# Performance work log

Hardware: AMD Instinct MI355X
Metric: run time of the kernel (lower is better)

## Reference

```python
import jax, jax.numpy as jnp
import numpy as np

B, F, L, P, H = 32, 64, 8192, 96, 8
HD = F // H
EPS_ATTN = 1e-6
EPS_REVIN = 1e-5
EPS_LN = 1e-5


def setup_inputs() -> dict:
    key = jax.random.key(0)
    ks = jax.random.split(key, 8)
    f32 = jnp.float32
    return {
        'x': jax.random.normal(ks[0], (B, F, L), dtype=f32),
        'gamma': jnp.ones((1, 1, F), dtype=f32),
        'beta': jnp.zeros((1, 1, F), dtype=f32),
        'ln_w': jnp.ones((F,), dtype=f32),
        'ln_b': jnp.zeros((F,), dtype=f32),
        'Wq': 0.05 * jax.random.normal(ks[1], (F, F), dtype=f32),
        'bq': jnp.zeros((F,), dtype=f32),
        'Wk': 0.05 * jax.random.normal(ks[2], (F, F), dtype=f32),
        'bk': jnp.zeros((F,), dtype=f32),
        'Wv': 0.05 * jax.random.normal(ks[3], (F, F), dtype=f32),
        'bv': jnp.zeros((F,), dtype=f32),
        'Wo': 0.05 * jax.random.normal(ks[4], (F, F), dtype=f32),
        'bo': jnp.zeros((F,), dtype=f32),
        'Wlin': 0.01 * jax.random.normal(ks[5], (P, L), dtype=f32),
        'blin': jnp.zeros((P,), dtype=f32),
        'Wp': 0.1 * jax.random.normal(ks[6], (1, F), dtype=f32),
        'bp': jnp.zeros((1,), dtype=f32),
    }


def _phi(t):
    # feature map: elu(x) + 1 (non-negative)
    return jax.nn.elu(t) + 1.0


def _layernorm(h, w, b):
    mu = jnp.mean(h, axis=-1, keepdims=True)
    var = jnp.mean(jnp.square(h - mu), axis=-1, keepdims=True)
    return (h - mu) * jax.lax.rsqrt(var + EPS_LN) * w + b


def reference(x, gamma, beta, ln_w, ln_b, Wq, bq, Wk, bk, Wv, bv, Wo, bo,
              Wlin, blin, Wp, bp):
    # (B, F, L) -> (B, L, F)
    xt = jnp.transpose(x, (0, 2, 1))
    # RevIN norm (stats over time axis, detached; torch std is unbiased ddof=1)
    mean = jax.lax.stop_gradient(jnp.mean(xt, axis=1, keepdims=True))
    std = jax.lax.stop_gradient(jnp.std(xt, axis=1, keepdims=True, ddof=1) + EPS_REVIN)
    xn = (xt - mean) / std * gamma + beta
    residual = xn
    h = _layernorm(xn, ln_w, ln_b)
    # Q/K/V projections (torch Linear: h @ W.T + b)
    Q = h @ Wq.T + bq
    K = h @ Wk.T + bk
    V = h @ Wv.T + bv
    # (B, L, F) -> (B, H, L, HD)
    def heads(t):
        return jnp.transpose(t.reshape(B, L, H, HD), (0, 2, 1, 3))
    Q, K, V = heads(Q), heads(K), heads(V)
    Q, K = _phi(Q), _phi(K)
    # linear attention: phi(Q) (phi(K)^T V) / (phi(Q) sum_n phi(K))
    KV = jnp.einsum('bhnd,bhne->bhde', K, V)           # (B,H,HD,HD)
    out = jnp.einsum('bhnd,bhde->bhne', Q, KV)          # (B,H,L,HD)
    Z = jnp.sum(K, axis=2)                              # (B,H,HD)
    normalizer = jnp.einsum('bhnd,bhd->bhn', Q, Z)[..., None] + EPS_ATTN
    out = out / normalizer
    out = jnp.transpose(out, (0, 2, 1, 3)).reshape(B, L, F)
    out = out @ Wo.T + bo
    y = out + residual                                  # (B, L, F)
    # temporal linear: (B, F, L) @ Wlin.T -> (B, F, P) -> (B, P, F)
    y = jnp.transpose(jnp.transpose(y, (0, 2, 1)) @ Wlin.T + blin, (0, 2, 1))
    # RevIN denorm
    y = (y - beta) / gamma
    y = y * std + mean
    # projector to scalar per step
    return (y @ Wp.T + bp)[..., 0]                      # (B, P)
```

## Files before the change

### kernel.cpp

```cpp
#include <hip/hip_runtime.h>
#include <cstddef>

#define NB 32
#define NF 64
#define NL 8192
#define NP 96
#define NH 8
#define TSPLIT 16

#define WS_MEAN 0
#define WS_STD  2048
#define WS_RSTD 4096
#define WS_KV   6144
#define WS_Z    22528
#define WS_OUT2 24576
#define WS_MUN  221184
#define WS_RSN  483328
#define WS_WLB  745472
#define WS_XNB  1138688
#define WS_YT   9527296
#define WS_XB   17915904

typedef __bf16 bfx8 __attribute__((ext_vector_type(8)));
typedef float f32x4 __attribute__((ext_vector_type(4)));
#define MFMA16(a, b, c) __builtin_amdgcn_mfma_f32_16x16x32_bf16((a), (b), (c), 0, 0, 0)

__device__ __forceinline__ unsigned short f2bf(float f) {
  unsigned u = __float_as_uint(f);
  unsigned r = u + 0x7FFFu + ((u >> 16) & 1u);
  return (unsigned short)(r >> 16);
}
__device__ __forceinline__ unsigned packbf2(float lo, float hi) {
  return (unsigned)f2bf(lo) | ((unsigned)f2bf(hi) << 16);
}
__device__ __forceinline__ float bflo(unsigned d) { return __uint_as_float(d << 16); }
__device__ __forceinline__ float bfhi(unsigned d) { return __uint_as_float(d & 0xFFFF0000u); }
__device__ __forceinline__ float bf1(unsigned short s) { return __uint_as_float(((unsigned)s) << 16); }

__device__ __forceinline__ bfx8 ldfrag(const unsigned short* p) {
  uint4 u = *(const uint4*)p;
  return __builtin_bit_cast(bfx8, u);
}

__global__ __launch_bounds__(256) void k_stats(const float* __restrict__ x,
                                               float* __restrict__ wmean,
                                               float* __restrict__ wstd,
                                               float* __restrict__ wrstd,
                                               unsigned short* __restrict__ xb) {
  int bf = blockIdx.x;
  int tid = threadIdx.x;
  const float4* row4 = (const float4*)(x + (size_t)bf * NL);
  unsigned short* xrow = xb + (size_t)bf * NL;
  float s1 = 0.f, s2 = 0.f;
#pragma unroll
  for (int i = 0; i < NL / 4 / 256; i++) {
    float4 v = row4[tid + i * 256];
    s1 += v.x + v.y + v.z + v.w;
    s2 += v.x * v.x + v.y * v.y + v.z * v.z + v.w * v.w;
    uint2 o;
    o.x = packbf2(v.x, v.y);
    o.y = packbf2(v.z, v.w);
    *(uint2*)&xrow[(tid + i * 256) * 4] = o;
  }
  __shared__ float r1[256], r2[256];
  r1[tid] = s1; r2[tid] = s2;
  __syncthreads();
  for (int off = 128; off > 0; off >>= 1) {
    if (tid < off) { r1[tid] += r1[tid + off]; r2[tid] += r2[tid + off]; }
    __syncthreads();
  }
  if (tid == 0) {
    float m = r1[0] * (1.f / NL);
    float var = (r2[0] - (float)NL * m * m) * (1.f / (NL - 1));
    float sd = sqrtf(fmaxf(var, 0.f)) + 1e-5f;
    wmean[bf] = m;
    wstd[bf] = sd;
    wrstd[bf] = 1.f / sd;
  }
}

__global__ __launch_bounds__(256) void k_wlb(const float* __restrict__ Wlin,
                                             unsigned short* __restrict__ wlb) {
  int i = blockIdx.x * 256 + threadIdx.x;
  int p = i >> 10;
  int l8 = (i & 1023) * 8;
  float4 va = *(const float4*)&Wlin[(size_t)p * NL + l8];
  float4 vb = *(const float4*)&Wlin[(size_t)p * NL + l8 + 4];
  uint4 o;
  o.x = packbf2(va.x, va.y); o.y = packbf2(va.z, va.w);
  o.z = packbf2(vb.x, vb.y); o.w = packbf2(vb.z, vb.w);
  *(uint4*)&wlb[(((size_t)(l8 >> 5)) * NP + p) * 32 + (l8 & 31)] = o;
}

__global__ __launch_bounds__(256, 4) void k_kv(
    const unsigned short* __restrict__ xb,
    const float* __restrict__ gamma, const float* __restrict__ beta,
    const float* __restrict__ lnw, const float* __restrict__ lnb,
    const float* __restrict__ Wk, const float* __restrict__ bk,
    const float* __restrict__ Wv, const float* __restrict__ bv,
    const float* __restrict__ wmean, const float* __restrict__ wrstd,
    float* __restrict__ wKV, float* __restrict__ wZ,
    float* __restrict__ wmun, float* __restrict__ wrsn,
    unsigned short* __restrict__ xnb) {
  __shared__ __align__(16) char smem[40960];
  unsigned short* hA  = (unsigned short*)smem;
  unsigned short* WkB = (unsigned short*)(smem + 18432);
  unsigned short* WvB = (unsigned short*)(smem + 27648);
  unsigned short* pK  = (unsigned short*)smem;
  unsigned short* pV  = (unsigned short*)(smem + 17408);
  float* SkT   = (float*)(smem + 36864);
  float* mun   = (float*)(smem + 37888);
  float* rsn   = (float*)(smem + 38400);
  float* pmom  = (float*)(smem + 38912);

  const int tid = threadIdx.x;
  const int b = blockIdx.x >> 6;
  const int tI = blockIdx.x & 63;
  const int L0 = tI * 128;
  const int lane = tid & 63, wv = tid >> 6;
  const int mm = lane & 15, qd = lane >> 4;

  {
    int jj = tid >> 2, g = tid & 3;
    int f0 = g * 16;
    float tkp = 0.f, tvp = 0.f;
#pragma unroll
    for (int i = 0; i < 4; i++) {
      int f = f0 + i * 4;
      float4 wk4 = *(const float4*)&Wk[jj * NF + f];
      float4 wv4 = *(const float4*)&Wv[jj * NF + f];
      float4 lw  = *(const float4*)&lnw[f];
      float4 lb  = *(const float4*)&lnb[f];
      uint2 pk2, pv2;
      pk2.x = packbf2(wk4.x * lw.x, wk4.y * lw.y);
      pk2.y = packbf2(wk4.z * lw.z, wk4.w * lw.w);
      pv2.x = packbf2(wv4.x * lw.x, wv4.y * lw.y);
      pv2.y = packbf2(wv4.z * lw.z, wv4.w * lw.w);
      *(uint2*)&WkB[jj * 72 + f] = pk2;
      *(uint2*)&WvB[jj * 72 + f] = pv2;
      tkp += lb.x * wk4.x + lb.y * wk4.y + lb.z * wk4.z + lb.w * wk4.w;
      tvp += lb.x * wv4.x + lb.y * wv4.y + lb.z * wv4.z + lb.w * wv4.w;
    }
    tkp += __shfl_xor(tkp, 1, 64); tkp += __shfl_xor(tkp, 2, 64);
    tvp += __shfl_xor(tvp, 1, 64); tvp += __shfl_xor(tvp, 2, 64);
    if (g == 0) {
      SkT[64 + jj]  = tkp + bk[jj];
      SkT[192 + jj] = tvp + bv[jj];
    }
  }

  {
    const int sel = tid >> 7;
    const int l = tid & 127;
    const int fbase = sel * 32;
    float s1 = 0.f, s2 = 0.f;
    float xn2[32];
#pragma unroll
    for (int i = 0; i < 32; i++) {
      int f = fbase + i;
      float v = bf1(xb[((size_t)(b * NF + f)) * NL + L0 + l]);
      v = (v - wmean[b * NF + f]) * wrstd[b * NF + f] * gamma[f] + beta[f];
      xn2[i] = v; s1 += v; s2 += v * v;
    }
    pmom[sel * 256 + l * 2] = s1;
    pmom[sel * 256 + l * 2 + 1] = s2;
    unsigned* hrow = (unsigned*)&hA[l * 72];
#pragma unroll
    for (int i = 0; i < 16; i++)
      hrow[fbase / 2 + i] = packbf2(xn2[2 * i], xn2[2 * i + 1]);
  }
  __syncthreads();

  if (tid < 128) {
    float s1 = pmom[tid * 2] + pmom[256 + tid * 2];
    float s2 = pmom[tid * 2 + 1] + pmom[256 + tid * 2 + 1];
    float mu = s1 * (1.f / NF);
    float var = s2 * (1.f / NF) - mu * mu;
    float rs = rsqrtf(fmaxf(var, 0.f) + 1e-5f);
    mun[tid] = mu; rsn[tid] = rs;
    wmun[(size_t)b * NL + L0 + tid] = mu;
    wrsn[(size_t)b * NL + L0 + tid] = rs;
  } else {
    int sel = (tid >> 6) - 2, j = tid & 63;
    const unsigned* wr = (const unsigned*)((sel ? WvB : WkB) + j * 72);
    float s = 0.f;
#pragma unroll
    for (int i = 0; i < 32; i++) { unsigned d = wr[i]; s += bflo(d) + bfhi(d); }
    SkT[sel * 128 + j] = s;
  }

  {
    int row = tid >> 1, half = tid & 1;
    const uint4* s4 = (const uint4*)&hA[row * 72 + half * 32];
    uint4* d4 = (uint4*)(xnb + (((size_t)(b * 64 + tI) * 128 + row) * 64 + half * 32));
    d4[0] = s4[0]; d4[1] = s4[1]; d4[2] = s4[2]; d4[3] = s4[3];
  }
  __syncthreads();

  const f32x4 fz = {0.f, 0.f, 0.f, 0.f};
  f32x4 kacc[2][4], vacc[2][4];
#pragma unroll
  for (int i = 0; i < 2; i++)
#pragma unroll
    for (int jt = 0; jt < 4; jt++) { kacc[i][jt] = fz; vacc[i][jt] = fz; }

#pragma unroll
  for (int kc = 0; kc < 2; kc++) {
    bfx8 a0 = ldfrag(&hA[(wv * 32 + mm) * 72 + kc * 32 + qd * 8]);
    bfx8 a1 = ldfrag(&hA[(wv * 32 + 16 + mm) * 72 + kc * 32 + qd * 8]);
#pragma unroll
    for (int jt = 0; jt < 4; jt++) {
      bfx8 bkf = ldfrag(&WkB[(jt * 16 + mm) * 72 + kc * 32 + qd * 8]);
      bfx8 bvf = ldfrag(&WvB[(jt * 16 + mm) * 72 + kc * 32 + qd * 8]);
      kacc[0][jt] = MFMA16(a0, bkf, kacc[0][jt]);
      kacc[1][jt] = MFMA16(a1, bkf, kacc[1][jt]);
      vacc[0][jt] = MFMA16(a0, bvf, vacc[0][jt]);
      vacc[1][jt] = MFMA16(a1, bvf, vacc[1][jt]);
    }
  }

#pragma unroll
  for (int lt2 = 0; lt2 < 2; lt2++) {
    float4 mu4 = *(const float4*)&mun[wv * 32 + lt2 * 16 + qd * 4];
    float4 rs4 = *(const float4*)&rsn[wv * 32 + lt2 * 16 + qd * 4];
    float muv[4] = {mu4.x, mu4.y, mu4.z, mu4.w};
    float rsv[4] = {rs4.x, rs4.y, rs4.z, rs4.w};
#pragma unroll
    for (int jt = 0; jt < 4; jt++) {
      int j = jt * 16 + mm;
      float Sk = SkT[j], Tk = SkT[64 + j], Sv = SkT[128 + j], Tv = SkT[192 + j];
#pragma unroll
      for (int r = 0; r < 4; r++) {
        float kk = rsv[r] * (kacc[lt2][jt][r] - muv[r] * Sk) + Tk;
        kacc[lt2][jt][r] = (kk > 0.f) ? (kk + 1.f) : __expf(kk);
        vacc[lt2][jt][r] = rsv[r] * (vacc[lt2][jt][r] - muv[r] * Sv) + Tv;
      }
    }
  }
  __syncthreads();

#pragma unroll
  for (int lt2 = 0; lt2 < 2; lt2++) {
    int l0 = wv * 32 + lt2 * 16 + qd * 4;
#pragma unroll
    for (int jt = 0; jt < 4; jt++) {
      int j = jt * 16 + mm;
      uint2 dk, dv;
      dk.x = packbf2(kacc[lt2][jt][0], kacc[lt2][jt][1]);
      dk.y = packbf2(kacc[lt2][jt][2], kacc[lt2][jt][3]);
      dv.x = packbf2(vacc[lt2][jt][0], vacc[lt2][jt][1]);
      dv.y = packbf2(vacc[lt2][jt][2], vacc[lt2][jt][3]);
      *(uint2*)&pK[j * 136 + l0] = dk;
      *(uint2*)&pV[j * 136 + l0] = dv;
    }
  }
  __syncthreads();

  {
    f32x4 racc = fz;
#pragma unroll
    for (int kb = 0; kb < 4; kb++) {
      bfx8 ak = ldfrag(&pK[(wv * 16 + mm) * 136 + kb * 32 + qd * 8]);
      bfx8 bv8 = ldfrag(&pV[(wv * 16 + mm) * 136 + kb * 32 + qd * 8]);
      racc = MFMA16(ak, bv8, racc);
    }
    int eh = mm >> 3, e = mm & 7;
#pragma unroll
    for (int r = 0; r < 4; r++) {
      int row = qd * 4 + r;
      if ((row >> 3) == eh)
        atomicAdd(&wKV[(b * NH + wv * 2 + eh) * 64 + (row & 7) * 8 + e], racc[r]);
    }
  }
  if (tid < 64) {
    const unsigned* kr = (const unsigned*)&pK[tid * 136];
    float zs = 0.f;
#pragma unroll
    for (int i = 0; i < 64; i++) { unsigned d = kr[i]; zs += bflo(d) + bfhi(d); }
    atomicAdd(&wZ[b * 64 + tid], zs);
  }
}

__global__ __launch_bounds__(256, 4) void k_qy(
    const unsigned short* __restrict__ xnb,
    const float* __restrict__ lnw, const float* __restrict__ lnb,
    const float* __restrict__ Wq, const float* __restrict__ bq,
    const float* __restrict__ Wo, const float* __restrict__ bo,
    const float* __restrict__ wmun, const float* __restrict__ wrsn,
    const float* __restrict__ wKV, const float* __restrict__ wZ,
    unsigned short* __restrict__ ytb) {
  __shared__ __align__(16) char smem[40704];
  unsigned short* hA  = (unsigned short*)smem;
  unsigned short* qaA = (unsigned short*)smem;
  unsigned short* WqB = (unsigned short*)(smem + 18432);
  unsigned short* WoB = (unsigned short*)(smem + 27648);
  float* kvz   = (float*)(smem + 36864);
  float* mun   = (float*)(smem + 39168);
  float* rsn   = (float*)(smem + 39680);
  float* SqTq  = (float*)(smem + 40192);

  const int tid = threadIdx.x;
  const int b = blockIdx.x >> 6;
  const int tI = blockIdx.x & 63;
  const int L0 = tI * 128;
  const int lane = tid & 63, wv = tid >> 6;
  const int mm = lane & 15, qd = lane >> 4;
  const unsigned short* xtile = xnb + (size_t)(b * 64 + tI) * 128 * 64;

  {
    int jj = tid >> 2, g = tid & 3;
    int f0 = g * 16;
    float tqp = 0.f;
#pragma unroll
    for (int i = 0; i < 4; i++) {
      int f = f0 + i * 4;
      float4 wq4 = *(const float4*)&Wq[jj * NF + f];
      float4 wo4 = *(const float4*)&Wo[jj * NF + f];
      float4 lw  = *(const float4*)&lnw[f];
      float4 lb  = *(const float4*)&lnb[f];
      uint2 pq2, po2;
      pq2.x = packbf2(wq4.x * lw.x, wq4.y * lw.y);
      pq2.y = packbf2(wq4.z * lw.z, wq4.w * lw.w);
      po2.x = packbf2(wo4.x, wo4.y);
      po2.y = packbf2(wo4.z, wo4.w);
      *(uint2*)&WqB[jj * 72 + f] = pq2;
      *(uint2*)&WoB[jj * 72 + f] = po2;
      tqp += lb.x * wq4.x + lb.y * wq4.y + lb.z * wq4.z + lb.w * wq4.w;
    }
    tqp += __shfl_xor(tqp, 1, 64); tqp += __shfl_xor(tqp, 2, 64);
    if (g == 0) SqTq[64 + jj] = tqp + bq[jj];
  }
  for (int i = tid; i < 576; i += 256)
    kvz[i] = (i < 512) ? wKV[b * 512 + i] : wZ[b * 64 + i - 512];
  {
    int row = tid >> 1, half = tid & 1;
    const uint4* s4 = (const uint4*)(xtile + (size_t)row * 64 + half * 32);
    uint4 u0 = s4[0], u1 = s4[1], u2 = s4[2], u3 = s4[3];
    uint4* d4 = (uint4*)&hA[row * 72 + half * 32];
    d4[0] = u0; d4[1] = u1; d4[2] = u2; d4[3] = u3;
  }
  if (tid < 128) {
    mun[tid] = wmun[(size_t)b * NL + L0 + tid];
    rsn[tid] = wrsn[(size_t)b * NL + L0 + tid];
  }
  __syncthreads();

  if (tid < 64) {
    const unsigned* wr = (const unsigned*)(WqB + tid * 72);
    float s = 0.f;
#pragma unroll
    for (int i = 0; i < 32; i++) { unsigned d = wr[i]; s += bflo(d) + bfhi(d); }
    SqTq[tid] = s;
  }
  __syncthreads();

  const f32x4 fz = {0.f, 0.f, 0.f, 0.f};

  {
    f32x4 qacc[2][4];
#pragma unroll
    for (int i = 0; i < 2; i++)
#pragma unroll
      for (int jt = 0; jt < 4; jt++) qacc[i][jt] = fz;
#pragma unroll
    for (int kc = 0; kc < 2; kc++) {
      bfx8 a0 = ldfrag(&hA[(wv * 32 + mm) * 72 + kc * 32 + qd * 8]);
      bfx8 a1 = ldfrag(&hA[(wv * 32 + 16 + mm) * 72 + kc * 32 + qd * 8]);
#pragma unroll
      for (int jt = 0; jt < 4; jt++) {
        bfx8 bqf = ldfrag(&WqB[(jt * 16 + mm) * 72 + kc * 32 + qd * 8]);
        qacc[0][jt] = MFMA16(a0, bqf, qacc[0][jt]);
        qacc[1][jt] = MFMA16(a1, bqf, qacc[1][jt]);
      }
    }
#pragma unroll
    for (int lt2 = 0; lt2 < 2; lt2++) {
      float4 mu4 = *(const float4*)&mun[wv * 32 + lt2 * 16 + qd * 4];
      float4 rs4 = *(const float4*)&rsn[wv * 32 + lt2 * 16 + qd * 4];
      float muv[4] = {mu4.x, mu4.y, mu4.z, mu4.w};
      float rsv[4] = {rs4.x, rs4.y, rs4.z, rs4.w};
      int l0 = wv * 32 + lt2 * 16 + qd * 4;
#pragma unroll
      for (int jt = 0; jt < 4; jt++) {
        int j = jt * 16 + mm;
        float Sj = SqTq[j], Tj = SqTq[64 + j];
#pragma unroll
        for (int r = 0; r < 4; r++) {
          float q = rsv[r] * (qacc[lt2][jt][r] - muv[r] * Sj) + Tj;
          q = (q > 0.f) ? (q + 1.f) : __expf(q);
          qaA[(l0 + r) * 72 + j] = f2bf(q);
        }
      }
    }
  }
  __syncthreads();

  {
    int lt = tid & 31, hd = tid >> 5;
    int lbase = lt * 4;
    float qv[4][8];
#pragma unroll
    for (int i = 0; i < 4; i++) {
      uint4 u = *(const uint4*)&qaA[(lbase + i) * 72 + hd * 8];
      qv[i][0] = bflo(u.x); qv[i][1] = bfhi(u.x);
      qv[i][2] = bflo(u.y); qv[i][3] = bfhi(u.y);
      qv[i][4] = bflo(u.z); qv[i][5] = bfhi(u.z);
      qv[i][6] = bflo(u.w); qv[i][7] = bfhi(u.w);
    }
    float att[4][8], nrm[4];
#pragma unroll
    for (int i = 0; i < 4; i++) {
      nrm[i] = 1e-6f;
#pragma unroll
      for (int e = 0; e < 8; e++) att[i][e] = 0.f;
    }
#pragma unroll
    for (int d = 0; d < 8; d++) {
      float zd = kvz[512 + hd * 8 + d];
      float4 kva = *(const float4*)&kvz[hd * 64 + d * 8];
      float4 kvb = *(const float4*)&kvz[hd * 64 + d * 8 + 4];
#pragma unroll
      for (int i = 0; i < 4; i++) {
        float qq = qv[i][d];
        nrm[i] = fmaf(qq, zd, nrm[i]);
        att[i][0] = fmaf(qq, kva.x, att[i][0]);
        att[i][1] = fmaf(qq, kva.y, att[i][1]);
        att[i][2] = fmaf(qq, kva.z, att[i][2]);
        att[i][3] = fmaf(qq, kva.w, att[i][3]);
        att[i][4] = fmaf(qq, kvb.x, att[i][4]);
        att[i][5] = fmaf(qq, kvb.y, att[i][5]);
        att[i][6] = fmaf(qq, kvb.z, att[i][6]);
        att[i][7] = fmaf(qq, kvb.w, att[i][7]);
      }
    }
#pragma unroll
    for (int i = 0; i < 4; i++) {
      float inv = 1.f / nrm[i];
      uint4 o;
      o.x = packbf2(att[i][0] * inv, att[i][1] * inv);
      o.y = packbf2(att[i][2] * inv, att[i][3] * inv);
      o.z = packbf2(att[i][4] * inv, att[i][5] * inv);
      o.w = packbf2(att[i][6] * inv, att[i][7] * inv);
      *(uint4*)&qaA[(lbase + i) * 72 + hd * 8] = o;
    }
  }
  __syncthreads();

  {
    f32x4 yacc[2][4];
#pragma unroll
    for (int i = 0; i < 2; i++)
#pragma unroll
      for (int ft = 0; ft < 4; ft++) yacc[i][ft] = fz;
#pragma unroll
    for (int ec = 0; ec < 2; ec++) {
      bfx8 a0 = ldfrag(&qaA[(wv * 32 + mm) * 72 + ec * 32 + qd * 8]);
      bfx8 a1 = ldfrag(&qaA[(wv * 32 + 16 + mm) * 72 + ec * 32 + qd * 8]);
#pragma unroll
      for (int ft = 0; ft < 4; ft++) {
        bfx8 bof = ldfrag(&WoB[(ft * 16 + mm) * 72 + ec * 32 + qd * 8]);
        yacc[0][ft] = MFMA16(a0, bof, yacc[0][ft]);
        yacc[1][ft] = MFMA16(a1, bof, yacc[1][ft]);
      }
    }
#pragma unroll
    for (int lt2 = 0; lt2 < 2; lt2++) {
      int l0 = wv * 32 + lt2 * 16 + qd * 4;
#pragma unroll
      for (int ft = 0; ft < 4; ft++) {
        int ff = ft * 16 + mm;
        float bof = bo[ff];
        float v0 = yacc[lt2][ft][0] + bf1(xtile[(size_t)(l0 + 0) * 64 + ff]) + bof;
        float v1 = yacc[lt2][ft][1] + bf1(xtile[(size_t)(l0 + 1) * 64 + ff]) + bof;
        float v2 = yacc[lt2][ft][2] + bf1(xtile[(size_t)(l0 + 2) * 64 + ff]) + bof;
        float v3 = yacc[lt2][ft][3] + bf1(xtile[(size_t)(l0 + 3) * 64 + ff]) + bof;
        uint2 o2;
        o2.x = packbf2(v0, v1);
        o2.y = packbf2(v2, v3);
        size_t idx = (((size_t)b * (NL / 32) + (L0 >> 5) + wv) * 64 + ff) * 32 + lt2 * 16 + qd * 4;
        *(uint2*)&ytb[idx] = o2;
      }
    }
  }
}

__global__ __launch_bounds__(256) void k_temporal(
    const unsigned short* __restrict__ ytb, const unsigned short* __restrict__ wlb,
    float* __restrict__ out2) {
  const int tid = threadIdx.x, lane = tid & 63, wvx = tid >> 6;
  const int mm = lane & 15, qd = lane >> 4;
  const int b = blockIdx.x / TSPLIT;
  const int kc = blockIdx.x % TSPLIT;
  const f32x4 fz = {0.f, 0.f, 0.f, 0.f};
  f32x4 acc[6];
#pragma unroll
  for (int pt = 0; pt < 6; pt++) acc[pt] = fz;

#pragma unroll 2
  for (int ks = 0; ks < (NL / 32) / TSPLIT; ks++) {
    int lg = kc * ((NL / 32) / TSPLIT) + ks;
    bfx8 bfr = ldfrag(&ytb[(((size_t)b * (NL / 32) + lg) * 64 + wvx * 16 + mm) * 32 + qd * 8]);
#pragma unroll
    for (int pt = 0; pt < 6; pt++) {
      bfx8 afr = ldfrag(&wlb[((size_t)lg * NP + pt * 16 + mm) * 32 + qd * 8]);
      acc[pt] = MFMA16(afr, bfr, acc[pt]);
    }
  }
  const int ff = wvx * 16 + mm;
#pragma unroll
  for (int pt = 0; pt < 6; pt++) {
#pragma unroll
    for (int r = 0; r < 4; r++) {
      int p = pt * 16 + qd * 4 + r;
      atomicAdd(&out2[((size_t)(b * NP + p)) * NF + ff], acc[pt][r]);
    }
  }
}

__global__ __launch_bounds__(64) void k_final(
    const float* __restrict__ out2, const float* __restrict__ blin,
    const float* __restrict__ gamma, const float* __restrict__ beta,
    const float* __restrict__ wmean, const float* __restrict__ wstd,
    const float* __restrict__ Wp, const float* __restrict__ bp,
    float* __restrict__ out) {
  int b = blockIdx.x / NP;
  int p = blockIdx.x % NP;
  int f = threadIdx.x;
  float v = out2[((size_t)(b * NP + p)) * NF + f] + blin[p];
  v = (v - beta[f]) / gamma[f];
  v = v * wstd[b * NF + f] + wmean[b * NF + f];
  float s = v * Wp[f];
#pragma unroll
  for (int off = 32; off > 0; off >>= 1)
    s += __shfl_down(s, off, 64);
  if (f == 0) out[blockIdx.x] = s + bp[0];
}

extern "C" void kernel_launch(void* const* d_in, const int* in_sizes, int n_in,
                              void* d_out, int out_size, void* d_ws, size_t ws_size,
                              hipStream_t stream) {
  const float* x     = (const float*)d_in[0];
  const float* gamma = (const float*)d_in[1];
  const float* beta  = (const float*)d_in[2];
  const float* lnw   = (const float*)d_in[3];
  const float* lnb   = (const float*)d_in[4];
  const float* Wq    = (const float*)d_in[5];
  const float* bq    = (const float*)d_in[6];
  const float* Wk    = (const float*)d_in[7];
  const float* bk    = (const float*)d_in[8];
  const float* Wv    = (const float*)d_in[9];
  const float* bv    = (const float*)d_in[10];
  const float* Wo    = (const float*)d_in[11];
  const float* bo    = (const float*)d_in[12];
  const float* Wlin  = (const float*)d_in[13];
  const float* blin  = (const float*)d_in[14];
  const float* Wp    = (const float*)d_in[15];
  const float* bp    = (const float*)d_in[16];
  float* out = (float*)d_out;
  float* ws  = (float*)d_ws;

  float* wmean = ws + WS_MEAN;
  float* wstd  = ws + WS_STD;
  float* wrstd = ws + WS_RSTD;
  float* wKV   = ws + WS_KV;
  float* wZ    = ws + WS_Z;
  float* wout2 = ws + WS_OUT2;
  float* wmun  = ws + WS_MUN;
  float* wrsn  = ws + WS_RSN;
  unsigned short* wlb = (unsigned short*)(ws + WS_WLB);
  unsigned short* xnb = (unsigned short*)(ws + WS_XNB);
  unsigned short* ytb = (unsigned short*)(ws + WS_YT);
  unsigned short* xb  = (unsigned short*)(ws + WS_XB);

  (void)hipMemsetAsync(wKV, 0, (size_t)(16384 + 2048 + 196608) * sizeof(float), stream);

  k_stats<<<NB * NF, 256, 0, stream>>>(x, wmean, wstd, wrstd, xb);
  k_wlb<<<NP * NL / 8 / 256, 256, 0, stream>>>(Wlin, wlb);
  k_kv<<<NB * 64, 256, 0, stream>>>(xb, gamma, beta, lnw, lnb, Wk, bk, Wv, bv,
                                    wmean, wrstd, wKV, wZ, wmun, wrsn, xnb);
  k_qy<<<NB * 64, 256, 0, stream>>>(xnb, lnw, lnb, Wq, bq, Wo, bo,
                                    wmun, wrsn, wKV, wZ, ytb);
  k_temporal<<<NB * TSPLIT, 256, 0, stream>>>(ytb, wlb, wout2);
  k_final<<<NB * NP, 64, 0, stream>>>(wout2, blin, gamma, beta, wmean, wstd, Wp, bp, out);
}
```

Measured before the change: 237.0 us.

## Fuse temporal projection and final denorm/projector into attention-output kernel

The temporal linear (Wlin) and the RevIN-denorm plus projector are now computed inside k_qy on each 128-step tile. Partial results are reduced across features with shuffles and atomically added into the output, which removes the ytb intermediate write/read and two kernel launches. The Wlin bf16 conversion is folded into k_stats as extra blocks. The k_kv input normalization is also restructured to load pairs of time steps and combine per-row moments with LDS atomics. The trade-off is many more global atomics on a small output (2048 blocks × 96 outputs) and extra memset/launch ordering work.

After: 274.9 us. 16.0% more time.

```diff
diff --git a/kernel.cpp b/kernel.cpp
--- a/kernel.cpp
+++ b/kernel.cpp
@@ -6,20 +6,17 @@
 #define NL 8192
 #define NP 96
 #define NH 8
-#define TSPLIT 16
 
 #define WS_MEAN 0
 #define WS_STD  2048
 #define WS_RSTD 4096
 #define WS_KV   6144
 #define WS_Z    22528
-#define WS_OUT2 24576
-#define WS_MUN  221184
-#define WS_RSN  483328
-#define WS_WLB  745472
-#define WS_XNB  1138688
-#define WS_YT   9527296
-#define WS_XB   17915904
+#define WS_MUN  24576
+#define WS_RSN  286720
+#define WS_WLB  548864
+#define WS_XNB  942080
+#define WS_XB   9330688
 
 typedef __bf16 bfx8 __attribute__((ext_vector_type(8)));
 typedef float f32x4 __attribute__((ext_vector_type(4)));
@@ -46,9 +43,23 @@
                                                float* __restrict__ wmean,
                                                float* __restrict__ wstd,
                                                float* __restrict__ wrstd,
-                                               unsigned short* __restrict__ xb) {
+                                               unsigned short* __restrict__ xb,
+                                               const float* __restrict__ Wlin,
+                                               unsigned short* __restrict__ wlb) {
+  int tid = threadIdx.x;
+  if (blockIdx.x >= NB * NF) {
+    int i = (blockIdx.x - NB * NF) * 256 + tid;
+    int p = i >> 10;
+    int l8 = (i & 1023) * 8;
+    float4 va = *(const float4*)&Wlin[(size_t)p * NL + l8];
+    float4 vb = *(const float4*)&Wlin[(size_t)p * NL + l8 + 4];
+    uint4 o;
+    o.x = packbf2(va.x, va.y); o.y = packbf2(va.z, va.w);
+    o.z = packbf2(vb.x, vb.y); o.w = packbf2(vb.z, vb.w);
+    *(uint4*)&wlb[(((size_t)(l8 >> 5)) * NP + p) * 32 + (l8 & 31)] = o;
+    return;
+  }
   int bf = blockIdx.x;
-  int tid = threadIdx.x;
   const float4* row4 = (const float4*)(x + (size_t)bf * NL);
   unsigned short* xrow = xb + (size_t)bf * NL;
   float s1 = 0.f, s2 = 0.f;
@@ -77,19 +88,6 @@
     wstd[bf] = sd;
     wrstd[bf] = 1.f / sd;
   }
-}
-
-__global__ __launch_bounds__(256) void k_wlb(const float* __restrict__ Wlin,
-                                             unsigned short* __restrict__ wlb) {
-  int i = blockIdx.x * 256 + threadIdx.x;
-  int p = i >> 10;
-  int l8 = (i & 1023) * 8;
-  float4 va = *(const float4*)&Wlin[(size_t)p * NL + l8];
-  float4 vb = *(const float4*)&Wlin[(size_t)p * NL + l8 + 4];
-  uint4 o;
-  o.x = packbf2(va.x, va.y); o.y = packbf2(va.z, va.w);
-  o.z = packbf2(vb.x, vb.y); o.w = packbf2(vb.z, vb.w);
-  *(uint4*)&wlb[(((size_t)(l8 >> 5)) * NP + p) * 32 + (l8 & 31)] = o;
 }
 
 __global__ __launch_bounds__(256, 4) void k_kv(
@@ -102,16 +100,14 @@
     float* __restrict__ wKV, float* __restrict__ wZ,
     float* __restrict__ wmun, float* __restrict__ wrsn,
     unsigned short* __restrict__ xnb) {
-  __shared__ __align__(16) char smem[40960];
+  __shared__ __align__(16) char smem[38912];
   unsigned short* hA  = (unsigned short*)smem;
   unsigned short* WkB = (unsigned short*)(smem + 18432);
   unsigned short* WvB = (unsigned short*)(smem + 27648);
   unsigned short* pK  = (unsigned short*)smem;
   unsigned short* pV  = (unsigned short*)(smem + 17408);
-  float* SkT   = (float*)(smem + 36864);
-  float* mun   = (float*)(smem + 37888);
-  float* rsn   = (float*)(smem + 38400);
-  float* pmom  = (float*)(smem + 38912);
+  float* SkT  = (float*)(smem + 36864);
+  float* pmom = (float*)(smem + 37888);
 
   const int tid = threadIdx.x;
   const int b = blockIdx.x >> 6;
@@ -120,6 +116,7 @@
   const int lane = tid & 63, wv = tid >> 6;
   const int mm = lane & 15, qd = lane >> 4;
 
+  pmom[tid & 255] = 0.f;
   {
     int jj = tid >> 2, g = tid & 3;
     int f0 = g * 16;
@@ -148,36 +145,46 @@
       SkT[192 + jj] = tvp + bv[jj];
     }
   }
-
-  {
-    const int sel = tid >> 7;
-    const int l = tid & 127;
-    const int fbase = sel * 32;
-    float s1 = 0.f, s2 = 0.f;
-    float xn2[32];
-#pragma unroll
-    for (int i = 0; i < 32; i++) {
-      int f = fbase + i;
-      float v = bf1(xb[((size_t)(b * NF + f)) * NL + L0 + l]);
-      v = (v - wmean[b * NF + f]) * wrstd[b * NF + f] * gamma[f] + beta[f];
-      xn2[i] = v; s1 += v; s2 += v * v;
-    }
-    pmom[sel * 256 + l * 2] = s1;
-    pmom[sel * 256 + l * 2 + 1] = s2;
-    unsigned* hrow = (unsigned*)&hA[l * 72];
-#pragma unroll
-    for (int i = 0; i < 16; i++)
-      hrow[fbase / 2 + i] = packbf2(xn2[2 * i], xn2[2 * i + 1]);
+  __syncthreads();
+
+  {
+    const int lt = tid & 63;
+    const int fg = tid >> 6;
+    const int lp = 2 * lt;
+    float s1a = 0.f, s2a = 0.f, s1b = 0.f, s2b = 0.f;
+    float xlo[16], xhi[16];
+#pragma unroll
+    for (int i = 0; i < 16; i++) {
+      int f = fg * 16 + i;
+      unsigned d = *(const unsigned*)&xb[((size_t)(b * NF + f)) * NL + L0 + lp];
+      float a = wrstd[b * NF + f] * gamma[f];
+      float c = beta[f] - wmean[b * NF + f] * a;
+      float v0 = fmaf(bflo(d), a, c);
+      float v1 = fmaf(bfhi(d), a, c);
+      xlo[i] = v0; xhi[i] = v1;
+      s1a += v0; s2a += v0 * v0;
+      s1b += v1; s2b += v1 * v1;
+    }
+    atomicAdd(&pmom[lp * 2], s1a);
+    atomicAdd(&pmom[lp * 2 + 1], s2a);
+    atomicAdd(&pmom[lp * 2 + 2], s1b);
+    atomicAdd(&pmom[lp * 2 + 3], s2b);
+    unsigned* r0 = (unsigned*)&hA[lp * 72 + fg * 16];
+    unsigned* r1 = (unsigned*)&hA[(lp + 1) * 72 + fg * 16];
+#pragma unroll
+    for (int i = 0; i < 8; i++) {
+      r0[i] = packbf2(xlo[2 * i], xlo[2 * i + 1]);
+      r1[i] = packbf2(xhi[2 * i], xhi[2 * i + 1]);
+    }
   }
   __syncthreads();
 
   if (tid < 128) {
-    float s1 = pmom[tid * 2] + pmom[256 + tid * 2];
-    float s2 = pmom[tid * 2 + 1] + pmom[256 + tid * 2 + 1];
+    float s1 = pmom[tid * 2], s2 = pmom[tid * 2 + 1];
     float mu = s1 * (1.f / NF);
     float var = s2 * (1.f / NF) - mu * mu;
     float rs = rsqrtf(fmaxf(var, 0.f) + 1e-5f);
-    mun[tid] = mu; rsn[tid] = rs;
+    pmom[tid * 2] = mu; pmom[tid * 2 + 1] = rs;
     wmun[(size_t)b * NL + L0 + tid] = mu;
     wrsn[(size_t)b * NL + L0 + tid] = rs;
   } else {
@@ -188,7 +195,6 @@
     for (int i = 0; i < 32; i++) { unsigned d = wr[i]; s += bflo(d) + bfhi(d); }
     SkT[sel * 128 + j] = s;
   }
-
   {
     int row = tid >> 1, half = tid & 1;
     const uint4* s4 = (const uint4*)&hA[row * 72 + half * 32];
@@ -221,10 +227,12 @@
 
 #pragma unroll
   for (int lt2 = 0; lt2 < 2; lt2++) {
-    float4 mu4 = *(const float4*)&mun[wv * 32 + lt2 * 16 + qd * 4];
-    float4 rs4 = *(const float4*)&rsn[wv * 32 + lt2 * 16 + qd * 4];
-    float muv[4] = {mu4.x, mu4.y, mu4.z, mu4.w};
-    float rsv[4] = {rs4.x, rs4.y, rs4.z, rs4.w};
+    float muv[4], rsv[4];
+#pragma unroll
+    for (int r = 0; r < 4; r++) {
+      float2 mr = *(const float2*)&pmom[(wv * 32 + lt2 * 16 + qd * 4 + r) * 2];
+      muv[r] = mr.x; rsv[r] = mr.y;
+    }
 #pragma unroll
     for (int jt = 0; jt < 4; jt++) {
       int j = jt * 16 + mm;
@@ -288,10 +296,16 @@
     const float* __restrict__ Wo, const float* __restrict__ bo,
     const float* __restrict__ wmun, const float* __restrict__ wrsn,
     const float* __restrict__ wKV, const float* __restrict__ wZ,
-    unsigned short* __restrict__ ytb) {
+    const unsigned short* __restrict__ wlb,
+    const float* __restrict__ wmean, const float* __restrict__ wstd,
+    const float* __restrict__ gamma, const float* __restrict__ beta,
+    const float* __restrict__ Wp, const float* __restrict__ blin,
+    const float* __restrict__ bp,
+    float* __restrict__ out) {
   __shared__ __align__(16) char smem[40704];
   unsigned short* hA  = (unsigned short*)smem;
   unsigned short* qaA = (unsigned short*)smem;
+  unsigned short* yF  = (unsigned short*)smem;
   unsigned short* WqB = (unsigned short*)(smem + 18432);
   unsigned short* WoB = (unsigned short*)(smem + 27648);
   float* kvz   = (float*)(smem + 36864);
@@ -446,94 +460,82 @@
   }
   __syncthreads();
 
-  {
-    f32x4 yacc[2][4];
-#pragma unroll
-    for (int i = 0; i < 2; i++)
-#pragma unroll
-      for (int ft = 0; ft < 4; ft++) yacc[i][ft] = fz;
-#pragma unroll
-    for (int ec = 0; ec < 2; ec++) {
-      bfx8 a0 = ldfrag(&qaA[(wv * 32 + mm) * 72 + ec * 32 + qd * 8]);
-      bfx8 a1 = ldfrag(&qaA[(wv * 32 + 16 + mm) * 72 + ec * 32 + qd * 8]);
-#pragma unroll
-      for (int ft = 0; ft < 4; ft++) {
-        bfx8 bof = ldfrag(&WoB[(ft * 16 + mm) * 72 + ec * 32 + qd * 8]);
-        yacc[0][ft] = MFMA16(a0, bof, yacc[0][ft]);
-        yacc[1][ft] = MFMA16(a1, bof, yacc[1][ft]);
+  f32x4 yacc[2][4];
+#pragma unroll
+  for (int i = 0; i < 2; i++)
+#pragma unroll
+    for (int ft = 0; ft < 4; ft++) yacc[i][ft] = fz;
+#pragma unroll
+  for (int ec = 0; ec < 2; ec++) {
+    bfx8 a0 = ldfrag(&qaA[(wv * 32 + mm) * 72 + ec * 32 + qd * 8]);
+    bfx8 a1 = ldfrag(&qaA[(wv * 32 + 16 + mm) * 72 + ec * 32 + qd * 8]);
+#pragma unroll
+    for (int ft = 0; ft < 4; ft++) {
+      bfx8 bof = ldfrag(&WoB[(ft * 16 + mm) * 72 + ec * 32 + qd * 8]);
+      yacc[0][ft] = MFMA16(a0, bof, yacc[0][ft]);
+      yacc[1][ft] = MFMA16(a1, bof, yacc[1][ft]);
+    }
+  }
+  __syncthreads();
+
+#pragma unroll
+  for (int lt2 = 0; lt2 < 2; lt2++) {
+    int l0 = wv * 32 + lt2 * 16 + qd * 4;
+#pragma unroll
+    for (int ft = 0; ft < 4; ft++) {
+      int ff = ft * 16 + mm;
+      float bof = bo[ff];
+      float v0 = yacc[lt2][ft][0] + bf1(xtile[(size_t)(l0 + 0) * 64 + ff]) + bof;
+      float v1 = yacc[lt2][ft][1] + bf1(xtile[(size_t)(l0 + 1) * 64 + ff]) + bof;
+      float v2 = yacc[lt2][ft][2] + bf1(xtile[(size_t)(l0 + 2) * 64 + ff]) + bof;
+      float v3 = yacc[lt2][ft][3] + bf1(xtile[(size_t)(l0 + 3) * 64 + ff]) + bof;
+      uint2 o2;
+      o2.x = packbf2(v0, v1);
+      o2.y = packbf2(v2, v3);
+      *(uint2*)&yF[ff * 136 + l0] = o2;
+    }
+  }
+  __syncthreads();
+
+  {
+    f32x4 tacc[6];
+#pragma unroll
+    for (int pt = 0; pt < 6; pt++) tacc[pt] = fz;
+#pragma unroll
+    for (int kb = 0; kb < 4; kb++) {
+      bfx8 bfr = ldfrag(&yF[(wv * 16 + mm) * 136 + kb * 32 + qd * 8]);
+      int lg = tI * 4 + kb;
+#pragma unroll
+      for (int pt = 0; pt < 6; pt++) {
+        bfx8 afr = ldfrag(&wlb[((size_t)lg * NP + pt * 16 + mm) * 32 + qd * 8]);
+        tacc[pt] = MFMA16(afr, bfr, tacc[pt]);
       }
     }
-#pragma unroll
-    for (int lt2 = 0; lt2 < 2; lt2++) {
-      int l0 = wv * 32 + lt2 * 16 + qd * 4;
-#pragma unroll
-      for (int ft = 0; ft < 4; ft++) {
-        int ff = ft * 16 + mm;
-        float bof = bo[ff];
-        float v0 = yacc[lt2][ft][0] + bf1(xtile[(size_t)(l0 + 0) * 64 + ff]) + bof;
-        float v1 = yacc[lt2][ft][1] + bf1(xtile[(size_t)(l0 + 1) * 64 + ff]) + bof;
-        float v2 = yacc[lt2][ft][2] + bf1(xtile[(size_t)(l0 + 2) * 64 + ff]) + bof;
-        float v3 = yacc[lt2][ft][3] + bf1(xtile[(size_t)(l0 + 3) * 64 + ff]) + bof;
-        uint2 o2;
-        o2.x = packbf2(v0, v1);
-        o2.y = packbf2(v2, v3);
-        size_t idx = (((size_t)b * (NL / 32) + (L0 >> 5) + wv) * 64 + ff) * 32 + lt2 * 16 + qd * 4;
-        *(uint2*)&ytb[idx] = o2;
+    int f = wv * 16 + mm;
+    float stdf = wstd[b * NF + f], gam = gamma[f], wpf = Wp[f];
+    float coef = wpf * stdf / gam;
+    float cc = wpf * (wmean[b * NF + f] - beta[f] * stdf / gam);
+    float S1p = coef, S2p = cc;
+    S1p += __shfl_xor(S1p, 1, 64); S1p += __shfl_xor(S1p, 2, 64);
+    S1p += __shfl_xor(S1p, 4, 64); S1p += __shfl_xor(S1p, 8, 64);
+    S2p += __shfl_xor(S2p, 1, 64); S2p += __shfl_xor(S2p, 2, 64);
+    S2p += __shfl_xor(S2p, 4, 64); S2p += __shfl_xor(S2p, 8, 64);
+#pragma unroll
+    for (int pt = 0; pt < 6; pt++) {
+#pragma unroll
+      for (int r = 0; r < 4; r++) {
+        float val = coef * tacc[pt][r];
+        val += __shfl_xor(val, 1, 64); val += __shfl_xor(val, 2, 64);
+        val += __shfl_xor(val, 4, 64); val += __shfl_xor(val, 8, 64);
+        int p = pt * 16 + qd * 4 + r;
+        if (tI == 0) {
+          val += blin[p] * S1p + S2p;
+          if (wv == 0) val += bp[0];
+        }
+        if (mm == 0) atomicAdd(&out[b * NP + p], val);
       }
     }
   }
-}
-
-__global__ __launch_bounds__(256) void k_temporal(
-    const unsigned short* __restrict__ ytb, const unsigned short* __restrict__ wlb,
-    float* __restrict__ out2) {
-  const int tid = threadIdx.x, lane = tid & 63, wvx = tid >> 6;
-  const int mm = lane & 15, qd = lane >> 4;
-  const int b = blockIdx.x / TSPLIT;
-  const int kc = blockIdx.x % TSPLIT;
-  const f32x4 fz = {0.f, 0.f, 0.f, 0.f};
-  f32x4 acc[6];
-#pragma unroll
-  for (int pt = 0; pt < 6; pt++) acc[pt] = fz;
-
-#pragma unroll 2
-  for (int ks = 0; ks < (NL / 32) / TSPLIT; ks++) {
-    int lg = kc * ((NL / 32) / TSPLIT) + ks;
-    bfx8 bfr = ldfrag(&ytb[(((size_t)b * (NL / 32) + lg) * 64 + wvx * 16 + mm) * 32 + qd * 8]);
-#pragma unroll
-    for (int pt = 0; pt < 6; pt++) {
-      bfx8 afr = ldfrag(&wlb[((size_t)lg * NP + pt * 16 + mm) * 32 + qd * 8]);
-      acc[pt] = MFMA16(afr, bfr, acc[pt]);
-    }
-  }
-  const int ff = wvx * 16 + mm;
-#pragma unroll
-  for (int pt = 0; pt < 6; pt++) {
-#pragma unroll
-    for (int r = 0; r < 4; r++) {
-      int p = pt * 16 + qd * 4 + r;
-      atomicAdd(&out2[((size_t)(b * NP + p)) * NF + ff], acc[pt][r]);
-    }
-  }
-}
-
-__global__ __launch_bounds__(64) void k_final(
-    const float* __restrict__ out2, const float* __restrict__ blin,
-    const float* __restrict__ gamma, const float* __restrict__ beta,
-    const float* __restrict__ wmean, const float* __restrict__ wstd,
-    const float* __restrict__ Wp, const float* __restrict__ bp,
-    float* __restrict__ out) {
-  int b = blockIdx.x / NP;
-  int p = blockIdx.x % NP;
-  int f = threadIdx.x;
-  float v = out2[((size_t)(b * NP + p)) * NF + f] + blin[p];
-  v = (v - beta[f]) / gamma[f];
-  v = v * wstd[b * NF + f] + wmean[b * NF + f];
-  float s = v * Wp[f];
-#pragma unroll
-  for (int off = 32; off > 0; off >>= 1)
-    s += __shfl_down(s, off, 64);
-  if (f == 0) out[blockIdx.x] = s + bp[0];
 }
 
 extern "C" void kernel_launch(void* const* d_in, const int* in_sizes, int n_in,
@@ -564,22 +566,20 @@
   float* wrstd = ws + WS_RSTD;
   float* wKV   = ws + WS_KV;
   float* wZ    = ws + WS_Z;
-  float* wout2 = ws + WS_OUT2;
   float* wmun  = ws + WS_MUN;
   float* wrsn  = ws + WS_RSN;
   unsigned short* wlb = (unsigned short*)(ws + WS_WLB);
   unsigned short* xnb = (unsigned short*)(ws + WS_XNB);
-  unsigned short* ytb = (unsigned short*)(ws + WS_YT);
   unsigned short* xb  = (unsigned short*)(ws + WS_XB);
 
-  (void)hipMemsetAsync(wKV, 0, (size_t)(16384 + 2048 + 196608) * sizeof(float), stream);
-
-  k_stats<<<NB * NF, 256, 0, stream>>>(x, wmean, wstd, wrstd, xb);
-  k_wlb<<<NP * NL / 8 / 256, 256, 0, stream>>>(Wlin, wlb);
+  (void)hipMemsetAsync(wKV, 0, (size_t)(16384 + 2048) * sizeof(float), stream);
+  (void)hipMemsetAsync(out, 0, (size_t)out_size * sizeof(float), stream);
+
+  k_stats<<<NB * NF + NP * NL / 8 / 256, 256, 0, stream>>>(x, wmean, wstd, wrstd, xb,
+                                                           Wlin, wlb);
   k_kv<<<NB * 64, 256, 0, stream>>>(xb, gamma, beta, lnw, lnb, Wk, bk, Wv, bv,
                                     wmean, wrstd, wKV, wZ, wmun, wrsn, xnb);
   k_qy<<<NB * 64, 256, 0, stream>>>(xnb, lnw, lnb, Wq, bq, Wo, bo,
-                                    wmun, wrsn, wKV, wZ, ytb);
-  k_temporal<<<NB * TSPLIT, 256, 0, stream>>>(ytb, wlb, wout2);
-  k_final<<<NB * NP, 64, 0, stream>>>(wout2, blin, gamma, beta, wmean, wstd, Wp, bp, out);
-}
+                                    wmun, wrsn, wKV, wZ, wlb,
+                                    wmean, wstd, gamma, beta, Wp, blin, bp, out);
+}
```
